# Optimization experiments

Hardware: AMD Instinct MI355X
Metric: run time of the kernel (lower is better)

The kernel has to match this reference:

```python
import jax, jax.numpy as jnp
import numpy as np


def setup_inputs() -> dict:
    key = jax.random.key(0)
    k1, k2, k3, k4 = jax.random.split(key, 4)
    B, H, S, D = 2, 16, 2048, 64
    q = jax.random.normal(k1, (B, H, S, D), dtype=jnp.float32)
    k = jax.random.normal(k2, (B, H, S, D), dtype=jnp.float32)
    v = jax.random.normal(k3, (B, H, S, D), dtype=jnp.float32)
    mask = jax.random.randint(k4, (1, 1, S, S), 0, 2, dtype=jnp.int32)
    return {"q": q, "k": k, "v": v, "mask": mask}


def reference(q, k, v, mask):
    # scores: [B,H,S,S] -- intentionally materialized as in the original
    d = k.shape[-1]
    scale = 1.0 / jnp.sqrt(jnp.asarray(d, dtype=q.dtype))
    x = jnp.einsum("bhqd,bhkd->bhqk", q, k) * scale
    x = x + mask.astype(x.dtype) * jnp.asarray(-10000.0, dtype=x.dtype)
    p = jax.nn.softmax(x, axis=-1)  # dropout is identity in eval mode
    return jnp.einsum("bhqk,bhkd->bhqd", p, v)
```

## Files before the change

### kernel.cpp

```cpp
#include <hip/hip_runtime.h>


#define S_LEN 2048
#define D_DIM 64
#define N_KT 32
#define LDK 72
#define LDV 72
#define TILE_SHORTS (64 * 72)
#define TILE_BYTES (TILE_SHORTS * 2)
#define NBH 32

typedef __attribute__((ext_vector_type(8))) short bf16x8;
typedef __attribute__((ext_vector_type(16))) float f32x16;
typedef __attribute__((ext_vector_type(2))) __fp16 fp16x2;
typedef unsigned int u32;
typedef unsigned long long u64;

#define C1 0.180336880111121f
#define CM (-14426.9504088896f)

static __device__ __forceinline__ unsigned short f2bf(float f) {
  union { float f; unsigned u; } x; x.f = f;
  return (unsigned short)((x.u + 0x8000u) >> 16);
}
static __device__ __forceinline__ unsigned packbf(float lo, float hi) {
  union { float f; unsigned u; } a, b; a.f = lo; b.f = hi;
  return ((a.u + 0x8000u) >> 16) | ((b.u + 0x8000u) & 0xffff0000u);
}
static __device__ __forceinline__ f32x16 zero16() {
  f32x16 z;
#pragma unroll
  for (int i = 0; i < 16; ++i) z[i] = 0.f;
  return z;
}
static __device__ __forceinline__ void dma16(const u32* g, u32* l) {
  __builtin_amdgcn_global_load_lds(
      (const __attribute__((address_space(1))) u32*)g,
      (__attribute__((address_space(3))) u32*)l, 16, 0, 0);
}
static __device__ __forceinline__ unsigned pkh(float lo, float hi) {
  union { fp16x2 h; unsigned u; } x;
  x.h = __builtin_amdgcn_cvt_pkrtz(lo, hi);
  return x.u;
}

__global__ __launch_bounds__(256) void prep_kv(
    const float* __restrict__ k, const float* __restrict__ v,
    unsigned short* __restrict__ kws, unsigned short* __restrict__ vws) {
  const int kt = blockIdx.x, bh = blockIdx.y;
  const int t = threadIdx.x;
  __shared__ unsigned short Vt[TILE_SHORTS];
  const size_t goff = (size_t)bh * (S_LEN * D_DIM) + (size_t)kt * 64 * D_DIM;
  const float4* kg = (const float4*)(k + goff);
  const float4* vg = (const float4*)(v + goff);
  unsigned short* kimg = kws + (size_t)(bh * N_KT + kt) * TILE_SHORTS;
#pragma unroll
  for (int j = 0; j < 4; ++j) {
    const int i = t + j * 256;
    const int row = i >> 4, c4 = i & 15;
    const float4 x = kg[i];
    ushort4 w;
    w.x = f2bf(x.x); w.y = f2bf(x.y); w.z = f2bf(x.z); w.w = f2bf(x.w);
    *(ushort4*)&kimg[row * LDK + c4 * 4] = w;
    const float4 y = vg[i];
    const int swc = 8 * (((row >> 3) + c4) & 7) + (row & 7);
    const unsigned p01 = pkh(y.x, y.y);
    const unsigned p23 = pkh(y.z, y.w);
    Vt[(4 * c4 + 0) * LDV + swc] = (unsigned short)(p01 & 0xffff);
    Vt[(4 * c4 + 1) * LDV + swc] = (unsigned short)(p01 >> 16);
    Vt[(4 * c4 + 2) * LDV + swc] = (unsigned short)(p23 & 0xffff);
    Vt[(4 * c4 + 3) * LDV + swc] = (unsigned short)(p23 >> 16);
  }
  __syncthreads();
  uint4* vimg = (uint4*)(vws + (size_t)(bh * N_KT + kt) * TILE_SHORTS);
  const uint4* lv = (const uint4*)Vt;
  for (int i = t; i < TILE_BYTES / 16; i += 256) vimg[i] = lv[i];
}

__global__ __launch_bounds__(256) void prep_mask(
    const int* __restrict__ mask, u32* __restrict__ mw) {
  const int wid = blockIdx.x * 4 + (threadIdx.x >> 6);
  const int lane = threadIdx.x & 63;
  const int row = wid >> 5, kt = wid & 31;
  const int mv = mask[(size_t)row * S_LEN + kt * 64 + lane];
  const u64 b = __ballot(mv != 0);
  if (lane < 32) {
    const int hl = lane >> 4, p = lane & 15;
    const int kb = p >> 3, g = (p >> 1) & 3, h = p & 1;
    const int j0 = 32 * kb + 8 * g + 4 * hl + 2 * h;
    u32 w = 0;
    if (!((b >> j0) & 1)) w |= 0x0000FFFFu;
    if (!((b >> (j0 + 1)) & 1)) w |= 0xFFFF0000u;
    mw[((size_t)(row * 2 + hl) * N_KT + kt) * 16 + p] = w;
  }
}

__global__ __launch_bounds__(128, 2) void attn_fwd(
    const float* __restrict__ q, const unsigned short* __restrict__ kws,
    const unsigned short* __restrict__ vws, const u32* __restrict__ mw,
    float* __restrict__ out) {
  const int qt = blockIdx.x;
  const int bh = blockIdx.y;
  const size_t hoff = (size_t)bh * (S_LEN * D_DIM);

  __shared__ unsigned short Ks[2][TILE_SHORTS];
  __shared__ unsigned short Vt[2][TILE_SHORTS];

  const int t = threadIdx.x;
  const int wave = t >> 6;
  const int lane = t & 63;
  const int col = lane & 31;
  const int hl = lane >> 5;
  const int sw = col >> 2;

  const int qg = qt * 64 + wave * 32 + col;

  bf16x8 bQ[4];
  {
    const float* qrow = q + hoff + (size_t)qg * D_DIM;
#pragma unroll
    for (int ks = 0; ks < 4; ++ks) {
      const float4 x0 = *(const float4*)(qrow + ks * 16 + hl * 8);
      const float4 x1 = *(const float4*)(qrow + ks * 16 + hl * 8 + 4);
      union { bf16x8 v; unsigned d[4]; } u;
      u.d[0] = packbf(x0.x * C1, x0.y * C1);
      u.d[1] = packbf(x0.z * C1, x0.w * C1);
      u.d[2] = packbf(x1.x * C1, x1.y * C1);
      u.d[3] = packbf(x1.z * C1, x1.w * C1);
      bQ[ks] = u.v;
    }
  }

  bf16x8 onesA;
  {
    union { bf16x8 v; unsigned d[4]; } u;
    u.d[0] = u.d[1] = u.d[2] = u.d[3] = 0x3C003C00u;
    onesA = u.v;
  }

  const unsigned short* kbase = kws + (size_t)bh * N_KT * TILE_SHORTS;
  const unsigned short* vbase = vws + (size_t)bh * N_KT * TILE_SHORTS;

  f32x16 oT0 = zero16(), oT1 = zero16(), oL = zero16();
  const uint4* mrow = (const uint4*)(mw + (size_t)(qg * 2 + hl) * N_KT * 16);

  {
    const u32* g = (const u32*)((wave == 0 ? kbase : vbase));
    u32* l = wave == 0 ? (u32*)&Ks[0][0] : (u32*)&Vt[0][0];
#pragma unroll
    for (int i = 0; i < 9; ++i) dma16(g + i * 256 + lane * 4, l + i * 256);
  }

  for (int kt = 0; kt < N_KT; ++kt) {
    __syncthreads();
    if (kt + 1 < N_KT) {
      const u32* g = (const u32*)((wave == 0 ? kbase : vbase) +
                                  (size_t)(kt + 1) * TILE_SHORTS);
      u32* l = wave == 0 ? (u32*)&Ks[(kt + 1) & 1][0]
                         : (u32*)&Vt[(kt + 1) & 1][0];
#pragma unroll
      for (int i = 0; i < 9; ++i) dma16(g + i * 256 + lane * 4, l + i * 256);
    }
    uint4 mq0 = mrow[kt * 4 + 0], mq1 = mrow[kt * 4 + 1];
    uint4 mq2 = mrow[kt * 4 + 2], mq3 = mrow[kt * 4 + 3];
    const u32 mwv[16] = {mq0.x, mq0.y, mq0.z, mq0.w, mq1.x, mq1.y, mq1.z, mq1.w,
                         mq2.x, mq2.y, mq2.z, mq2.w, mq3.x, mq3.y, mq3.z, mq3.w};
    const unsigned short* Ksb = Ks[kt & 1];
    const unsigned short* Vtb = Vt[kt & 1];

    f32x16 sT0 = zero16(), sT1 = zero16();
#pragma unroll
    for (int ks = 0; ks < 4; ++ks) {
      const bf16x8 aK0 = *(const bf16x8*)&Ksb[col * LDK + ks * 16 + hl * 8];
      const bf16x8 aK1 = *(const bf16x8*)&Ksb[(32 + col) * LDK + ks * 16 + hl * 8];
      sT0 = __builtin_amdgcn_mfma_f32_32x32x16_bf16(aK0, bQ[ks], sT0, 0, 0, 0);
      sT1 = __builtin_amdgcn_mfma_f32_32x32x16_bf16(aK1, bQ[ks], sT1, 0, 0, 0);
    }

    unsigned pw[16];
#pragma unroll
    for (int kb = 0; kb < 2; ++kb) {
      const f32x16 sT = kb ? sT1 : sT0;
#pragma unroll
      for (int g = 0; g < 4; ++g) {
        const float e0 = __builtin_amdgcn_exp2f(sT[g * 4 + 0]);
        const float e1 = __builtin_amdgcn_exp2f(sT[g * 4 + 1]);
        const float e2 = __builtin_amdgcn_exp2f(sT[g * 4 + 2]);
        const float e3 = __builtin_amdgcn_exp2f(sT[g * 4 + 3]);
        pw[kb * 8 + g * 2 + 0] = pkh(e0, e1) & mwv[kb * 8 + g * 2 + 0];
        pw[kb * 8 + g * 2 + 1] = pkh(e2, e3) & mwv[kb * 8 + g * 2 + 1];
      }
    }

#pragma unroll
    for (int ks = 0; ks < 4; ++ks) {
      const int kb = ks >> 1, h = ks & 1;
      const unsigned d0 = pw[kb * 8 + 4 * h + 0], d1 = pw[kb * 8 + 4 * h + 1];
      const unsigned d2 = pw[kb * 8 + 4 * h + 2], d3 = pw[kb * 8 + 4 * h + 3];
      const unsigned s0 = hl ? d0 : d2;
      const unsigned s1 = hl ? d1 : d3;
      const unsigned r0 = (unsigned)__shfl_xor((int)s0, 32);
      const unsigned r1 = (unsigned)__shfl_xor((int)s1, 32);
      union { bf16x8 v; unsigned d[4]; } pf;
      pf.d[0] = hl ? r0 : d0;
      pf.d[1] = hl ? r1 : d1;
      pf.d[2] = hl ? d2 : r0;
      pf.d[3] = hl ? d3 : r1;
      const int cpr = 8 * (((2 * ks + hl) + sw) & 7);
      const bf16x8 aV0 = *(const bf16x8*)&Vtb[col * LDV + cpr];
      const bf16x8 aV1 = *(const bf16x8*)&Vtb[(32 + col) * LDV + cpr];
      oT0 = __builtin_amdgcn_mfma_f32_32x32x16_f16(aV0, pf.v, oT0, 0, 0, 0);
      oT1 = __builtin_amdgcn_mfma_f32_32x32x16_f16(aV1, pf.v, oT1, 0, 0, 0);
      oL = __builtin_amdgcn_mfma_f32_32x32x16_f16(onesA, pf.v, oL, 0, 0, 0);
    }
  }

  const float inv = 1.0f / oL[0];
  float* orow = out + hoff + (size_t)qg * D_DIM;
#pragma unroll
  for (int rg = 0; rg < 4; ++rg) {
    float4 w0, w1;
    w0.x = oT0[rg * 4 + 0] * inv; w0.y = oT0[rg * 4 + 1] * inv;
    w0.z = oT0[rg * 4 + 2] * inv; w0.w = oT0[rg * 4 + 3] * inv;
    w1.x = oT1[rg * 4 + 0] * inv; w1.y = oT1[rg * 4 + 1] * inv;
    w1.z = oT1[rg * 4 + 2] * inv; w1.w = oT1[rg * 4 + 3] * inv;
    *(float4*)(orow + 8 * rg + 4 * hl) = w0;
    *(float4*)(orow + 32 + 8 * rg + 4 * hl) = w1;
  }
}

__global__ __launch_bounds__(256, 2) void attn_fwd_self(
    const float* __restrict__ q, const float* __restrict__ k,
    const float* __restrict__ v, const int* __restrict__ mask,
    float* __restrict__ out) {
  const int qt = blockIdx.x;
  const int bh = blockIdx.y;
  const size_t hoff = (size_t)bh * (S_LEN * D_DIM);
  __shared__ unsigned short Ks[64 * LDK];
  __shared__ unsigned short Vt[64 * LDV];
  const int t = threadIdx.x;
  const int wave = t >> 6;
  const int lane = t & 63;
  const int col = lane & 31;
  const int hl = lane >> 5;
  const int sw = col >> 2;
  const int qg = qt * 128 + wave * 32 + col;
  bf16x8 bQ[4];
  {
    const float* qrow = q + hoff + (size_t)qg * D_DIM;
#pragma unroll
    for (int ks = 0; ks < 4; ++ks) {
      const float4 x0 = *(const float4*)(qrow + ks * 16 + hl * 8);
      const float4 x1 = *(const float4*)(qrow + ks * 16 + hl * 8 + 4);
      union { bf16x8 v; unsigned d[4]; } u;
      u.d[0] = packbf(x0.x, x0.y);
      u.d[1] = packbf(x0.z, x0.w);
      u.d[2] = packbf(x1.x, x1.y);
      u.d[3] = packbf(x1.z, x1.w);
      bQ[ks] = u.v;
    }
  }
  float4 pk[4], pv[4];
  {
    const float4* kg = (const float4*)(k + hoff);
    const float4* vg = (const float4*)(v + hoff);
#pragma unroll
    for (int j = 0; j < 4; ++j) { pk[j] = kg[t + j * 256]; pv[j] = vg[t + j * 256]; }
  }
  f32x16 oT0 = zero16(), oT1 = zero16();
  float lacc = 0.f;
  const int* mrow = mask + (size_t)qg * S_LEN;
  for (int kt = 0; kt < N_KT; ++kt) {
    __syncthreads();
#pragma unroll
    for (int j = 0; j < 4; ++j) {
      const int i = t + j * 256;
      const int row = i >> 4, c4 = i & 15;
      ushort4 w;
      w.x = f2bf(pk[j].x); w.y = f2bf(pk[j].y);
      w.z = f2bf(pk[j].z); w.w = f2bf(pk[j].w);
      *(ushort4*)&Ks[row * LDK + c4 * 4] = w;
      const int swc = 8 * (((row >> 3) + c4) & 7) + (row & 7);
      Vt[(4 * c4 + 0) * LDV + swc] = f2bf(pv[j].x);
      Vt[(4 * c4 + 1) * LDV + swc] = f2bf(pv[j].y);
      Vt[(4 * c4 + 2) * LDV + swc] = f2bf(pv[j].z);
      Vt[(4 * c4 + 3) * LDV + swc] = f2bf(pv[j].w);
    }
    __syncthreads();
    if (kt + 1 < N_KT) {
      const float4* kg = (const float4*)(k + hoff + (size_t)(kt + 1) * 64 * D_DIM);
      const float4* vg = (const float4*)(v + hoff + (size_t)(kt + 1) * 64 * D_DIM);
#pragma unroll
      for (int j = 0; j < 4; ++j) { pk[j] = kg[t + j * 256]; pv[j] = vg[t + j * 256]; }
    }
    int4 mq[2][4];
#pragma unroll
    for (int kb = 0; kb < 2; ++kb)
#pragma unroll
      for (int g = 0; g < 4; ++g)
        mq[kb][g] = *(const int4*)(mrow + kt * 64 + kb * 32 + g * 8 + hl * 4);
    f32x16 sT0 = zero16(), sT1 = zero16();
#pragma unroll
    for (int ks = 0; ks < 4; ++ks) {
      const bf16x8 aK0 = *(const bf16x8*)&Ks[col * LDK + ks * 16 + hl * 8];
      const bf16x8 aK1 = *(const bf16x8*)&Ks[(32 + col) * LDK + ks * 16 + hl * 8];
      sT0 = __builtin_amdgcn_mfma_f32_32x32x16_bf16(aK0, bQ[ks], sT0, 0, 0, 0);
      sT1 = __builtin_amdgcn_mfma_f32_32x32x16_bf16(aK1, bQ[ks], sT1, 0, 0, 0);
    }
    unsigned pw[2][8];
#pragma unroll
    for (int kb = 0; kb < 2; ++kb) {
      const f32x16 sT = kb ? sT1 : sT0;
      float e[16];
#pragma unroll
      for (int g = 0; g < 4; ++g) {
        const int4 mv = mq[kb][g];
        const int* mvp = &mv.x;
#pragma unroll
        for (int r3 = 0; r3 < 4; ++r3) {
          const int reg = g * 4 + r3;
          const float bias = mvp[r3] ? CM : 0.0f;
          const float ev = __builtin_amdgcn_exp2f(fmaf(sT[reg], C1, bias));
          e[reg] = ev;
          lacc += ev;
        }
        pw[kb][g * 2 + 0] = packbf(e[g * 4 + 0], e[g * 4 + 1]);
        pw[kb][g * 2 + 1] = packbf(e[g * 4 + 2], e[g * 4 + 3]);
      }
    }
#pragma unroll
    for (int ks = 0; ks < 4; ++ks) {
      const int kb = ks >> 1, h = ks & 1;
      const unsigned d0 = pw[kb][4 * h + 0], d1 = pw[kb][4 * h + 1];
      const unsigned d2 = pw[kb][4 * h + 2], d3 = pw[kb][4 * h + 3];
      const unsigned s0 = hl ? d0 : d2;
      const unsigned s1 = hl ? d1 : d3;
      const unsigned r0 = (unsigned)__shfl_xor((int)s0, 32);
      const unsigned r1 = (unsigned)__shfl_xor((int)s1, 32);
      union { bf16x8 v; unsigned d[4]; } pf;
      pf.d[0] = hl ? r0 : d0;
      pf.d[1] = hl ? r1 : d1;
      pf.d[2] = hl ? d2 : r0;
      pf.d[3] = hl ? d3 : r1;
      const int cpr = 8 * (((2 * ks + hl) + sw) & 7);
      const bf16x8 aV0 = *(const bf16x8*)&Vt[col * LDV + cpr];
      const bf16x8 aV1 = *(const bf16x8*)&Vt[(32 + col) * LDV + cpr];
      oT0 = __builtin_amdgcn_mfma_f32_32x32x16_bf16(aV0, pf.v, oT0, 0, 0, 0);
      oT1 = __builtin_amdgcn_mfma_f32_32x32x16_bf16(aV1, pf.v, oT1, 0, 0, 0);
    }
  }
  const float ltot = lacc + __shfl_xor(lacc, 32);
  const float inv = 1.0f / ltot;
  float* orow = out + hoff + (size_t)qg * D_DIM;
#pragma unroll
  for (int rg = 0; rg < 4; ++rg) {
    float4 w0, w1;
    w0.x = oT0[rg * 4 + 0] * inv; w0.y = oT0[rg * 4 + 1] * inv;
    w0.z = oT0[rg * 4 + 2] * inv; w0.w = oT0[rg * 4 + 3] * inv;
    w1.x = oT1[rg * 4 + 0] * inv; w1.y = oT1[rg * 4 + 1] * inv;
    w1.z = oT1[rg * 4 + 2] * inv; w1.w = oT1[rg * 4 + 3] * inv;
    *(float4*)(orow + 8 * rg + 4 * hl) = w0;
    *(float4*)(orow + 32 + 8 * rg + 4 * hl) = w1;
  }
}

extern "C" void kernel_launch(void* const* d_in, const int* in_sizes, int n_in,
                              void* d_out, int out_size, void* d_ws, size_t ws_size,
                              hipStream_t stream) {
  const float* q = (const float*)d_in[0];
  const float* k = (const float*)d_in[1];
  const float* v = (const float*)d_in[2];
  const int* mask = (const int*)d_in[3];
  float* out = (float*)d_out;

  const size_t img_elems = (size_t)NBH * N_KT * TILE_SHORTS;
  const size_t mw_words = (size_t)S_LEN * 2 * N_KT * 16;
  const size_t need = img_elems * 2 * sizeof(unsigned short) + mw_words * 4;

  if (ws_size >= need) {
    unsigned short* kws = (unsigned short*)d_ws;
    unsigned short* vws = kws + img_elems;
    u32* mwp = (u32*)(vws + img_elems);
    prep_kv<<<dim3(N_KT, NBH), dim3(256), 0, stream>>>(k, v, kws, vws);
    prep_mask<<<dim3((S_LEN * N_KT) / 4), dim3(256), 0, stream>>>(mask, mwp);
    attn_fwd<<<dim3(S_LEN / 64, NBH), dim3(128), 0, stream>>>(q, kws, vws, mwp, out);
  } else {
    attn_fwd_self<<<dim3(S_LEN / 128, NBH), dim3(256), 0, stream>>>(q, k, v, mask, out);
  }
}
```

Baseline: 168.8 us.

## Split key tile across two waves per query group and reduce partial outputs in LDS

```diff
diff --git a/kernel.cpp b/kernel.cpp
--- a/kernel.cpp
+++ b/kernel.cpp
@@ -95,7 +95,7 @@
   }
 }
 
-__global__ __launch_bounds__(128, 2) void attn_fwd(
+__global__ __launch_bounds__(256, 4) void attn_fwd(
     const float* __restrict__ q, const unsigned short* __restrict__ kws,
     const unsigned short* __restrict__ vws, const u32* __restrict__ mw,
     float* __restrict__ out) {
@@ -112,8 +112,10 @@
   const int col = lane & 31;
   const int hl = lane >> 5;
   const int sw = col >> 2;
-
-  const int qg = qt * 64 + wave * 32 + col;
+  const int qh = wave >> 1;
+  const int kh = wave & 1;
+
+  const int qg = qt * 64 + qh * 32 + col;
 
   bf16x8 bQ[4];
   {
@@ -145,58 +147,62 @@
   const uint4* mrow = (const uint4*)(mw + (size_t)(qg * 2 + hl) * N_KT * 16);
 
   {
-    const u32* g = (const u32*)((wave == 0 ? kbase : vbase));
-    u32* l = wave == 0 ? (u32*)&Ks[0][0] : (u32*)&Vt[0][0];
-#pragma unroll
-    for (int i = 0; i < 9; ++i) dma16(g + i * 256 + lane * 4, l + i * 256);
+    const u32* g = (const u32*)(qh == 0 ? kbase : vbase);
+    u32* l = qh == 0 ? (u32*)&Ks[0][0] : (u32*)&Vt[0][0];
+    if (!kh) {
+#pragma unroll
+      for (int i = 0; i < 5; ++i) dma16(g + i * 256 + lane * 4, l + i * 256);
+    } else {
+#pragma unroll
+      for (int i = 5; i < 9; ++i) dma16(g + i * 256 + lane * 4, l + i * 256);
+    }
   }
 
   for (int kt = 0; kt < N_KT; ++kt) {
     __syncthreads();
     if (kt + 1 < N_KT) {
-      const u32* g = (const u32*)((wave == 0 ? kbase : vbase) +
+      const u32* g = (const u32*)((qh == 0 ? kbase : vbase) +
                                   (size_t)(kt + 1) * TILE_SHORTS);
-      u32* l = wave == 0 ? (u32*)&Ks[(kt + 1) & 1][0]
-                         : (u32*)&Vt[(kt + 1) & 1][0];
-#pragma unroll
-      for (int i = 0; i < 9; ++i) dma16(g + i * 256 + lane * 4, l + i * 256);
-    }
-    uint4 mq0 = mrow[kt * 4 + 0], mq1 = mrow[kt * 4 + 1];
-    uint4 mq2 = mrow[kt * 4 + 2], mq3 = mrow[kt * 4 + 3];
-    const u32 mwv[16] = {mq0.x, mq0.y, mq0.z, mq0.w, mq1.x, mq1.y, mq1.z, mq1.w,
-                         mq2.x, mq2.y, mq2.z, mq2.w, mq3.x, mq3.y, mq3.z, mq3.w};
+      u32* l = qh == 0 ? (u32*)&Ks[(kt + 1) & 1][0]
+                       : (u32*)&Vt[(kt + 1) & 1][0];
+      if (!kh) {
+#pragma unroll
+        for (int i = 0; i < 5; ++i) dma16(g + i * 256 + lane * 4, l + i * 256);
+      } else {
+#pragma unroll
+        for (int i = 5; i < 9; ++i) dma16(g + i * 256 + lane * 4, l + i * 256);
+      }
+    }
+    const uint4 mq0 = mrow[kt * 4 + kh * 2 + 0];
+    const uint4 mq1 = mrow[kt * 4 + kh * 2 + 1];
+    const u32 mwv[8] = {mq0.x, mq0.y, mq0.z, mq0.w,
+                        mq1.x, mq1.y, mq1.z, mq1.w};
     const unsigned short* Ksb = Ks[kt & 1];
     const unsigned short* Vtb = Vt[kt & 1];
 
-    f32x16 sT0 = zero16(), sT1 = zero16();
+    f32x16 sT = zero16();
 #pragma unroll
     for (int ks = 0; ks < 4; ++ks) {
-      const bf16x8 aK0 = *(const bf16x8*)&Ksb[col * LDK + ks * 16 + hl * 8];
-      const bf16x8 aK1 = *(const bf16x8*)&Ksb[(32 + col) * LDK + ks * 16 + hl * 8];
-      sT0 = __builtin_amdgcn_mfma_f32_32x32x16_bf16(aK0, bQ[ks], sT0, 0, 0, 0);
-      sT1 = __builtin_amdgcn_mfma_f32_32x32x16_bf16(aK1, bQ[ks], sT1, 0, 0, 0);
-    }
-
-    unsigned pw[16];
-#pragma unroll
-    for (int kb = 0; kb < 2; ++kb) {
-      const f32x16 sT = kb ? sT1 : sT0;
-#pragma unroll
-      for (int g = 0; g < 4; ++g) {
-        const float e0 = __builtin_amdgcn_exp2f(sT[g * 4 + 0]);
-        const float e1 = __builtin_amdgcn_exp2f(sT[g * 4 + 1]);
-        const float e2 = __builtin_amdgcn_exp2f(sT[g * 4 + 2]);
-        const float e3 = __builtin_amdgcn_exp2f(sT[g * 4 + 3]);
-        pw[kb * 8 + g * 2 + 0] = pkh(e0, e1) & mwv[kb * 8 + g * 2 + 0];
-        pw[kb * 8 + g * 2 + 1] = pkh(e2, e3) & mwv[kb * 8 + g * 2 + 1];
-      }
-    }
-
-#pragma unroll
-    for (int ks = 0; ks < 4; ++ks) {
-      const int kb = ks >> 1, h = ks & 1;
-      const unsigned d0 = pw[kb * 8 + 4 * h + 0], d1 = pw[kb * 8 + 4 * h + 1];
-      const unsigned d2 = pw[kb * 8 + 4 * h + 2], d3 = pw[kb * 8 + 4 * h + 3];
+      const bf16x8 aK =
+          *(const bf16x8*)&Ksb[(kh * 32 + col) * LDK + ks * 16 + hl * 8];
+      sT = __builtin_amdgcn_mfma_f32_32x32x16_bf16(aK, bQ[ks], sT, 0, 0, 0);
+    }
+
+    unsigned pw[8];
+#pragma unroll
+    for (int g2 = 0; g2 < 4; ++g2) {
+      const float e0 = __builtin_amdgcn_exp2f(sT[g2 * 4 + 0]);
+      const float e1 = __builtin_amdgcn_exp2f(sT[g2 * 4 + 1]);
+      const float e2 = __builtin_amdgcn_exp2f(sT[g2 * 4 + 2]);
+      const float e3 = __builtin_amdgcn_exp2f(sT[g2 * 4 + 3]);
+      pw[g2 * 2 + 0] = pkh(e0, e1) & mwv[g2 * 2 + 0];
+      pw[g2 * 2 + 1] = pkh(e2, e3) & mwv[g2 * 2 + 1];
+    }
+
+#pragma unroll
+    for (int ks2 = 0; ks2 < 2; ++ks2) {
+      const unsigned d0 = pw[4 * ks2 + 0], d1 = pw[4 * ks2 + 1];
+      const unsigned d2 = pw[4 * ks2 + 2], d3 = pw[4 * ks2 + 3];
       const unsigned s0 = hl ? d0 : d2;
       const unsigned s1 = hl ? d1 : d3;
       const unsigned r0 = (unsigned)__shfl_xor((int)s0, 32);
@@ -206,7 +212,7 @@
       pf.d[1] = hl ? r1 : d1;
       pf.d[2] = hl ? d2 : r0;
       pf.d[3] = hl ? d3 : r1;
-      const int cpr = 8 * (((2 * ks + hl) + sw) & 7);
+      const int cpr = 8 * (((4 * kh + 2 * ks2 + hl) + sw) & 7);
       const bf16x8 aV0 = *(const bf16x8*)&Vtb[col * LDV + cpr];
       const bf16x8 aV1 = *(const bf16x8*)&Vtb[(32 + col) * LDV + cpr];
       oT0 = __builtin_amdgcn_mfma_f32_32x32x16_f16(aV0, pf.v, oT0, 0, 0, 0);
@@ -215,17 +221,45 @@
     }
   }
 
-  const float inv = 1.0f / oL[0];
-  float* orow = out + hoff + (size_t)qg * D_DIM;
-#pragma unroll
-  for (int rg = 0; rg < 4; ++rg) {
-    float4 w0, w1;
-    w0.x = oT0[rg * 4 + 0] * inv; w0.y = oT0[rg * 4 + 1] * inv;
-    w0.z = oT0[rg * 4 + 2] * inv; w0.w = oT0[rg * 4 + 3] * inv;
-    w1.x = oT1[rg * 4 + 0] * inv; w1.y = oT1[rg * 4 + 1] * inv;
-    w1.z = oT1[rg * 4 + 2] * inv; w1.w = oT1[rg * 4 + 3] * inv;
-    *(float4*)(orow + 8 * rg + 4 * hl) = w0;
-    *(float4*)(orow + 32 + 8 * rg + 4 * hl) = w1;
+  __syncthreads();
+  {
+    float* xb = (float*)&Ks[0][0];
+    float* lb = (float*)&Vt[0][0];
+    float* xr = xb + (size_t)(qh * 32 + col) * 68;
+    if (kh) {
+#pragma unroll
+      for (int rg = 0; rg < 4; ++rg) {
+        float4 w0, w1;
+        w0.x = oT0[rg * 4 + 0]; w0.y = oT0[rg * 4 + 1];
+        w0.z = oT0[rg * 4 + 2]; w0.w = oT0[rg * 4 + 3];
+        w1.x = oT1[rg * 4 + 0]; w1.y = oT1[rg * 4 + 1];
+        w1.z = oT1[rg * 4 + 2]; w1.w = oT1[rg * 4 + 3];
+        *(float4*)(xr + 8 * rg + 4 * hl) = w0;
+        *(float4*)(xr + 32 + 8 * rg + 4 * hl) = w1;
+      }
+      if (!hl) lb[qh * 32 + col] = oL[0];
+    }
+    __syncthreads();
+    if (!kh) {
+      const float inv = 1.0f / (oL[0] + lb[qh * 32 + col]);
+      float* orow = out + hoff + (size_t)qg * D_DIM;
+#pragma unroll
+      for (int rg = 0; rg < 4; ++rg) {
+        const float4 a0 = *(const float4*)(xr + 8 * rg + 4 * hl);
+        const float4 a1 = *(const float4*)(xr + 32 + 8 * rg + 4 * hl);
+        float4 w0, w1;
+        w0.x = (oT0[rg * 4 + 0] + a0.x) * inv;
+        w0.y = (oT0[rg * 4 + 1] + a0.y) * inv;
+        w0.z = (oT0[rg * 4 + 2] + a0.z) * inv;
+        w0.w = (oT0[rg * 4 + 3] + a0.w) * inv;
+        w1.x = (oT1[rg * 4 + 0] + a1.x) * inv;
+        w1.y = (oT1[rg * 4 + 1] + a1.y) * inv;
+        w1.z = (oT1[rg * 4 + 2] + a1.z) * inv;
+        w1.w = (oT1[rg * 4 + 3] + a1.w) * inv;
+        *(float4*)(orow + 8 * rg + 4 * hl) = w0;
+        *(float4*)(orow + 32 + 8 * rg + 4 * hl) = w1;
+      }
+    }
   }
 }
 
@@ -383,7 +417,7 @@
     u32* mwp = (u32*)(vws + img_elems);
     prep_kv<<<dim3(N_KT, NBH), dim3(256), 0, stream>>>(k, v, kws, vws);
     prep_mask<<<dim3((S_LEN * N_KT) / 4), dim3(256), 0, stream>>>(mask, mwp);
-    attn_fwd<<<dim3(S_LEN / 64, NBH), dim3(128), 0, stream>>>(q, kws, vws, mwp, out);
+    attn_fwd<<<dim3(S_LEN / 64, NBH), dim3(256), 0, stream>>>(q, kws, vws, mwp, out);
   } else {
     attn_fwd_self<<<dim3(S_LEN / 128, NBH), dim3(256), 0, stream>>>(q, k, v, mask, out);
   }
```

Result: slower. 177.9 us (+5.4%).
